# Performance work log

Measured on AMD Instinct MI355X. Metric: run time of the kernel, lower is better.

The kernel has to match this reference:

```python
import jax, jax.numpy as jnp
import numpy as np

H = 16  # n_heads
D = 1024  # embed_dim == input_dim
FF = 4 * D
EPS = 1e-5  # torch LayerNorm default


def layer_norm(x, g, b):
    m = x.mean(-1, keepdims=True)
    v = x.var(-1, keepdims=True)
    return (x - m) / jnp.sqrt(v + EPS) * g + b


def setup_inputs() -> dict:
    key = jax.random.key(0)
    ks = jax.random.split(key, 8)
    s = lambda k, sh: (jax.random.normal(k, sh, jnp.float32) * 0.02)
    return {
        "kq": jax.random.normal(ks[0], (4, 2048, 512), jnp.float32),
        "v": jax.random.normal(ks[1], (4, 2048, 512), jnp.float32),
        "Wk": s(ks[2], (D, D)), "bk": jnp.zeros((D,), jnp.float32),
        "Wq": s(ks[3], (D, D)), "bq": jnp.zeros((D,), jnp.float32),
        "Wv": s(ks[4], (D, D)), "bv": jnp.zeros((D,), jnp.float32),
        "W1": s(ks[5], (FF, D)), "b1": jnp.zeros((FF,), jnp.float32),
        "W2": s(ks[6], (D, FF)), "b2": jnp.zeros((D,), jnp.float32),
        "g1": jnp.ones((D,), jnp.float32), "be1": jnp.zeros((D,), jnp.float32),
        "g2": jnp.ones((D,), jnp.float32), "be2": jnp.zeros((D,), jnp.float32),
    }


def reference(kq, v, Wk, bk, Wq, bq, Wv, bv, W1, b1, W2, b2, g1, be1, g2, be2):
    X = jnp.concatenate([kq, v], axis=-1)  # [n, T, input_dim]
    n, T, _ = kq.shape

    def heads(y):  # [n, T, D] -> [n, H, T, hd]
        return y.reshape(n, T, H, -1).transpose(0, 2, 1, 3)

    K = heads(X @ Wk.T + bk)
    Q = heads(X @ Wq.T + bq)
    V = heads(X @ Wv.T + bv)

    # NOTE: source applies no 1/sqrt(head_dim) scaling
    scores = jnp.einsum('nhqd,nhkd->nhqk', Q, K)
    causal = jnp.tril(jnp.ones((T, T), bool))  # mask = -inf strictly above diagonal
    scores = jnp.where(causal, scores, -jnp.inf)
    A = jax.nn.softmax(scores, axis=-1)
    attn_out = jnp.einsum('nhqk,nhkd->nhqd', A, V)
    attn_out = attn_out.transpose(0, 2, 1, 3).reshape(n, T, -1)  # [n, T, D]

    Vflat = V.transpose(0, 2, 1, 3).reshape(n, T, -1)  # residual is V projection, per source
    h = layer_norm(Vflat + attn_out, g1, be1)
    ff = jax.nn.gelu(h @ W1.T + b1, approximate=False) @ W2.T + b2  # torch GELU default = exact erf
    return layer_norm(h + ff, g2, be2)
```

## Files before the change

### kernel.cpp

```cpp
#include <hip/hip_runtime.h>
#include <stdint.h>

#define SEQ 2048
#define DM  1024
#define NH  16
#define HD  64
#define FFD 4096
#define TOK 8192

typedef __bf16 bf16x8 __attribute__((ext_vector_type(8)));
typedef float  f32x4  __attribute__((ext_vector_type(4)));
typedef float  f32x16 __attribute__((ext_vector_type(16)));
typedef unsigned short u16x8 __attribute__((ext_vector_type(8)));
typedef unsigned short u16x4 __attribute__((ext_vector_type(4)));
typedef unsigned int   u32x4 __attribute__((ext_vector_type(4)));

__device__ __forceinline__ unsigned short f2bf(float f) {
  unsigned u = __builtin_bit_cast(unsigned, f);
  u += 0x7fffu + ((u >> 16) & 1u);
  return (unsigned short)(u >> 16);
}
__device__ __forceinline__ float bf2f(unsigned short h) {
  return __builtin_bit_cast(float, ((unsigned)h) << 16);
}
__device__ __forceinline__ f32x4 mfma16(bf16x8 a, bf16x8 b, f32x4 c) {
  return __builtin_amdgcn_mfma_f32_16x16x32_bf16(a, b, c, 0, 0, 0);
}
__device__ __forceinline__ f32x16 mfma32(bf16x8 a, bf16x8 b, f32x16 c) {
  return __builtin_amdgcn_mfma_f32_32x32x16_bf16(a, b, c, 0, 0, 0);
}
__device__ __forceinline__ unsigned cvtpk(float lo, float hi) {
  unsigned r;
  asm("v_cvt_pk_bf16_f32 %0, %1, %2" : "=v"(r) : "v"(lo), "v"(hi));
  return r;
}
__device__ __forceinline__ void gld_lds16(void* lds, const void* g) {
  __builtin_amdgcn_global_load_lds((__attribute__((address_space(1))) void*)g,
                                   (__attribute__((address_space(3))) void*)lds,
                                   16, 0, 0);
}

__global__ __launch_bounds__(256) void concat_cast(
    const float* __restrict__ kq, const float* __restrict__ v,
    unsigned short* __restrict__ X) {
  int i = (blockIdx.x * 256 + threadIdx.x) * 4;
  int tkn = i >> 10;
  int c = i & 1023;
  const float* s = (c < 512) ? (kq + (size_t)tkn * 512 + c)
                             : (v  + (size_t)tkn * 512 + (c - 512));
  f32x4 f = *(const f32x4*)s;
  u16x4 o = { f2bf(f[0]), f2bf(f[1]), f2bf(f[2]), f2bf(f[3]) };
  *(u16x4*)&X[i] = o;
}

__global__ __launch_bounds__(256) void castW5(
    const float* __restrict__ Wk, const float* __restrict__ Wq,
    const float* __restrict__ Wv, const float* __restrict__ W1,
    const float* __restrict__ W2, unsigned short* __restrict__ dst1,
    unsigned short* __restrict__ dst2) {
  int e = (blockIdx.x * 256 + threadIdx.x) * 4;
  const float* src;
  unsigned short* dst;
  if (e < 3145728) {
    src = (e < 1048576) ? (Wk + e)
        : (e < 2097152) ? (Wq + (e - 1048576))
                        : (Wv + (e - 2097152));
    dst = dst1 + e;
  } else {
    int e2 = e - 3145728;
    src = (e2 < 4194304) ? (W1 + e2) : (W2 + (e2 - 4194304));
    dst = dst2 + e2;
  }
  f32x4 f = *(const f32x4*)src;
  u16x4 o = { f2bf(f[0]), f2bf(f[1]), f2bf(f[2]), f2bf(f[3]) };
  *(u16x4*)dst = o;
}

__global__ __launch_bounds__(256) void bias3(
    const float* __restrict__ a, const float* __restrict__ b,
    const float* __restrict__ c, float* __restrict__ o) {
  int i = blockIdx.x * 256 + threadIdx.x;
  if (i < 1024) o[i] = a[i];
  else if (i < 2048) o[i] = b[i - 1024];
  else if (i < 3072) o[i] = c[i - 2048];
}

template<int BM, int EPI>
__global__ __launch_bounds__(512, 2) void gemm256(
    const unsigned short* __restrict__ A, const unsigned short* __restrict__ B,
    const float* __restrict__ bias, void* __restrict__ Cout,
    void* __restrict__ CoutQ, void* __restrict__ CoutV, void* __restrict__ CoutVI,
    int M, int N, int K, int PR, int PC, int NPC) {
  constexpr int MF = BM / 32;
  constexpr int MG = MF / 4;
  extern __shared__ __align__(16) unsigned short lds[];
  unsigned short* Asm0 = lds;
  unsigned short* Bsm0 = lds + 2 * BM * 64;
  const int tid = threadIdx.x;
  const int w = tid >> 6, l = tid & 63, lr = l & 15, lg = l >> 4;
  const int wm = w >> 2, wn = w & 3;
  const int bid = blockIdx.x;
  const int xcd = bid & 7;
  const int i = bid >> 3;
  const int patch_r = xcd / NPC, patch_c = xcd % NPC;
  const int bm = (patch_r * PR + (i % PR)) * BM;
  const int bn = (patch_c * PC + (i / PR)) * 256;
  const int NT = K >> 6;
  const int srow = tid >> 3;
  const int sc8  = tid & 7;

  f32x4 acc[MF][4] = {};

  auto stage = [&](int kt, int bb) {
    unsigned short* da = Asm0 + bb * (BM * 64);
    unsigned short* db = Bsm0 + bb * (256 * 64);
#pragma unroll
    for (int p = 0; p < BM / 64; ++p) {
      int row = p * 64 + srow;
      gld_lds16(da + (p * 512 + w * 64) * 8,
                &A[(size_t)(bm + row) * K + kt * 64 + ((sc8 ^ (row & 7)) << 3)]);
    }
#pragma unroll
    for (int p = 0; p < 4; ++p) {
      int row = p * 64 + srow;
      gld_lds16(db + (p * 512 + w * 64) * 8,
                &B[(size_t)(bn + row) * K + kt * 64 + ((sc8 ^ (row & 7)) << 3)]);
    }
  };

  stage(0, 0);

  for (int t = 0; t < NT; ++t) {
    asm volatile("s_waitcnt vmcnt(0)" ::: "memory");
    __builtin_amdgcn_s_barrier();
    if (t + 1 < NT) stage(t + 1, (t + 1) & 1);
    const unsigned short* As = Asm0 + (t & 1) * (BM * 64);
    const unsigned short* Bs = Bsm0 + (t & 1) * (256 * 64);
    bf16x8 bv[4][2];
#pragma unroll
    for (int fn = 0; fn < 4; ++fn)
#pragma unroll
      for (int kk = 0; kk < 2; ++kk) {
        int row = wn * 64 + fn * 16 + lr;
        int c8 = (kk * 4 + lg) ^ (row & 7);
        bv[fn][kk] = *(const bf16x8*)&Bs[row * 64 + c8 * 8];
      }
#pragma unroll
    for (int mg = 0; mg < MG; ++mg) {
      bf16x8 av[4][2];
#pragma unroll
      for (int fr = 0; fr < 4; ++fr)
#pragma unroll
        for (int kk = 0; kk < 2; ++kk) {
          int row = wm * (BM / 2) + (mg * 4 + fr) * 16 + lr;
          int c8 = (kk * 4 + lg) ^ (row & 7);
          av[fr][kk] = *(const bf16x8*)&As[row * 64 + c8 * 8];
        }
      __builtin_amdgcn_s_setprio(1);
#pragma unroll
      for (int fr = 0; fr < 4; ++fr)
#pragma unroll
        for (int nf = 0; nf < 4; ++nf)
#pragma unroll
          for (int kk = 0; kk < 2; ++kk)
            acc[mg * 4 + fr][nf] = mfma16(av[fr][kk], bv[nf][kk], acc[mg * 4 + fr][nf]);
      __builtin_amdgcn_s_setprio(0);
    }
  }
#pragma unroll
  for (int mf = 0; mf < MF; ++mf) {
    int row0 = bm + wm * (BM / 2) + mf * 16 + lg * 4;
#pragma unroll
    for (int nf = 0; nf < 4; ++nf) {
      int col = bn + wn * 64 + nf * 16 + lr;
      float bcol = bias[col];
#pragma unroll
      for (int r = 0; r < 4; ++r) {
        float vv = acc[mf][nf][r] + bcol;
        int row = row0 + r;
        if (EPI == 2) vv = 0.5f * vv * (1.0f + erff(vv * 0.70710678118654752f));
        if (EPI == 0) {
          ((float*)Cout)[(size_t)row * N + col] = vv;
        } else if (EPI == 5) {
          int third = col >> 10, c = col & 1023;
          unsigned short hv = f2bf(vv);
          int bb = row >> 11, tt = row & 2047;
          if (third == 0) {
            int hh = c >> 6, dc = (c >> 4) & 3, dl = c & 15;
            ((unsigned short*)Cout)[((((size_t)(bb * 16 + hh) * 4 + dc) * 2048 + tt) << 4) + dl] = hv;
          } else if (third == 1) {
            ((unsigned short*)CoutQ)[(size_t)row * 1024 + c] = hv;
          } else {
            ((unsigned short*)CoutV)[(size_t)row * 1024 + c] = hv;
            int hh = c >> 6, d = c & 63;
            ((unsigned short*)CoutVI)[((((size_t)(bb * 16 + hh) * 128 + (tt >> 4)) * 64 + d) << 4) + (tt & 15)] = hv;
          }
        } else {
          ((unsigned short*)Cout)[(size_t)row * N + col] = f2bf(vv);
        }
      }
    }
  }
}

__global__ __launch_bounds__(128, 4) void attn_kernel(
    const unsigned short* __restrict__ Q, const unsigned short* __restrict__ KI,
    const unsigned short* __restrict__ VI, unsigned short* __restrict__ O) {
  __shared__ __align__(16) unsigned short T[2][32 * 72];
  const int tid = threadIdx.x;
  const int w = tid >> 6, l = tid & 63;
  const int q32 = l & 31;
  const int g = l >> 5;
  const int x = blockIdx.x;
  const int bh = (x & 7) * 8 + (x >> 3);
  const int b = bh >> 4, h = bh & 15;
  const int u = 63 - (2 * (int)blockIdx.y + w);
  const size_t tok0 = (size_t)b * SEQ;
  const size_t hoff = (size_t)h * 64;
  const unsigned short* Kp = KI + (size_t)bh * 4 * SEQ * 16;
  const unsigned short* Vp = VI + (size_t)bh * 128 * 64 * 16;

  const int q0 = u * 32;
  const int qg = q0 + q32;

  bf16x8 qf[4];
#pragma unroll
  for (int ks = 0; ks < 4; ++ks)
    qf[ks] = *(const bf16x8*)&Q[(tok0 + qg) * DM + hoff + ks * 16 + g * 8];

  f32x16 ot0 = {}, ot1 = {};
  float m = -3.0e38f, lden = 0.f;

  bf16x8 kf[4], vf[4];
#pragma unroll
  for (int ks = 0; ks < 4; ++ks)
    kf[ks] = *(const bf16x8*)&Kp[((size_t)ks * SEQ + q32) * 16 + g * 8];
#pragma unroll
  for (int dt = 0; dt < 2; ++dt)
#pragma unroll
    for (int s = 0; s < 2; ++s)
      vf[dt * 2 + s] = *(const bf16x8*)&Vp[((size_t)s * 64 + dt * 32 + q32) * 16 + g * 8];

#pragma unroll 1
  for (int j = 0; j <= u; ++j) {
    f32x16 st = {};
    __builtin_amdgcn_s_setprio(1);
#pragma unroll
    for (int ks = 0; ks < 4; ++ks) st = mfma32(kf[ks], qf[ks], st);
    __builtin_amdgcn_s_setprio(0);
    const int jn = (j < u) ? j + 1 : u;
    bf16x8 kn[4], vn[4];
#pragma unroll
    for (int ks = 0; ks < 4; ++ks)
      kn[ks] = *(const bf16x8*)&Kp[((size_t)ks * SEQ + jn * 32 + q32) * 16 + g * 8];
#pragma unroll
    for (int dt = 0; dt < 2; ++dt)
#pragma unroll
      for (int s = 0; s < 2; ++s)
        vn[dt * 2 + s] = *(const bf16x8*)&Vp[(((size_t)jn * 2 + s) * 64 + dt * 32 + q32) * 16 + g * 8];
    if (j == u) {
#pragma unroll
      for (int r = 0; r < 16; ++r) {
        int kg = j * 32 + (r & 3) + 8 * (r >> 2) + 4 * g;
        if (kg > qg) st[r] = -3.0e38f;
      }
    }
    float x0 = fmaxf(st[0], st[1]),  x1 = fmaxf(st[2], st[3]);
    float x2 = fmaxf(st[4], st[5]),  x3 = fmaxf(st[6], st[7]);
    float x4 = fmaxf(st[8], st[9]),  x5 = fmaxf(st[10], st[11]);
    float x6 = fmaxf(st[12], st[13]), x7 = fmaxf(st[14], st[15]);
    x0 = fmaxf(x0, x1); x2 = fmaxf(x2, x3); x4 = fmaxf(x4, x5); x6 = fmaxf(x6, x7);
    x0 = fmaxf(x0, x2); x4 = fmaxf(x4, x6);
    float pmax = fmaxf(x0, x4);
    if (__any(pmax - m > 8.0f)) {
      float pp = fmaxf(pmax, __shfl_xor(pmax, 32, 64));
      float mnew = fmaxf(m, pp);
      float sc = __expf(m - mnew);
#pragma unroll
      for (int r = 0; r < 16; ++r) { ot0[r] *= sc; ot1[r] *= sc; }
      lden *= sc;
      m = mnew;
    }
    float p[16];
#pragma unroll
    for (int r = 0; r < 16; ++r) p[r] = __expf(st[r] - m);
    {
      float s0 = p[0] + p[1], s1 = p[2] + p[3], s2 = p[4] + p[5], s3 = p[6] + p[7];
      float s4 = p[8] + p[9], s5 = p[10] + p[11], s6 = p[12] + p[13], s7 = p[14] + p[15];
      s0 += s1; s2 += s3; s4 += s5; s6 += s7;
      s0 += s2; s4 += s6;
      lden += s0 + s4;
    }
    unsigned c0 = cvtpk(p[0], p[1]),   c1 = cvtpk(p[2], p[3]);
    unsigned c2 = cvtpk(p[4], p[5]),   c3 = cvtpk(p[6], p[7]);
    unsigned c4 = cvtpk(p[8], p[9]),   c5 = cvtpk(p[10], p[11]);
    unsigned c6 = cvtpk(p[12], p[13]), c7 = cvtpk(p[14], p[15]);
    unsigned y0 = __shfl_xor(c0, 32, 64), y1 = __shfl_xor(c1, 32, 64);
    unsigned y2 = __shfl_xor(c2, 32, 64), y3 = __shfl_xor(c3, 32, 64);
    unsigned y4 = __shfl_xor(c4, 32, 64), y5 = __shfl_xor(c5, 32, 64);
    unsigned y6 = __shfl_xor(c6, 32, 64), y7 = __shfl_xor(c7, 32, 64);
    u32x4 f0 = { g ? y2 : c0, g ? y3 : c1, g ? c2 : y0, g ? c3 : y1 };
    u32x4 f1 = { g ? y6 : c4, g ? y7 : c5, g ? c6 : y4, g ? c7 : y5 };
    bf16x8 pb0 = __builtin_bit_cast(bf16x8, f0);
    bf16x8 pb1 = __builtin_bit_cast(bf16x8, f1);
    __builtin_amdgcn_s_setprio(1);
    ot0 = mfma32(vf[0], pb0, ot0);
    ot0 = mfma32(vf[1], pb1, ot0);
    ot1 = mfma32(vf[2], pb0, ot1);
    ot1 = mfma32(vf[3], pb1, ot1);
    __builtin_amdgcn_s_setprio(0);
#pragma unroll
    for (int ks = 0; ks < 4; ++ks) kf[ks] = kn[ks];
#pragma unroll
    for (int q = 0; q < 4; ++q) vf[q] = vn[q];
  }
  lden += __shfl_xor(lden, 32, 64);
  float inv = 1.0f / lden;
#pragma unroll
  for (int r = 0; r < 16; ++r) {
    int d = (r & 3) + 8 * (r >> 2) + 4 * g;
    T[w][q32 * 72 + d]      = f2bf(ot0[r] * inv);
    T[w][q32 * 72 + 32 + d] = f2bf(ot1[r] * inv);
  }
#pragma unroll
  for (int j2 = 0; j2 < 4; ++j2) {
    int col = g * 32 + j2 * 8;
    u16x8 vv = *(const u16x8*)&T[w][q32 * 72 + col];
    *(u16x8*)&O[(tok0 + q0 + q32) * DM + hoff + col] = vv;
  }
}

template<int MODE>
__global__ __launch_bounds__(256) void ln_kernel(
    const unsigned short* __restrict__ Xa, const void* __restrict__ Xc,
    const float* __restrict__ g, const float* __restrict__ be,
    void* __restrict__ outp) {
  const int row = blockIdx.x, t = threadIdx.x;
  const size_t base = (size_t)row * DM + t * 4;
  float x[4];
  u16x4 a = *(const u16x4*)&Xa[base];
  if (MODE == 0) {
    u16x4 c = *(const u16x4*)&((const unsigned short*)Xc)[base];
#pragma unroll
    for (int i = 0; i < 4; ++i) x[i] = bf2f(a[i]) + bf2f(c[i]);
  } else {
    f32x4 c = *(const f32x4*)&((const float*)Xc)[base];
#pragma unroll
    for (int i = 0; i < 4; ++i) x[i] = bf2f(a[i]) + c[i];
  }
  float s = x[0] + x[1] + x[2] + x[3];
  float ss = x[0] * x[0] + x[1] * x[1] + x[2] * x[2] + x[3] * x[3];
#pragma unroll
  for (int m = 1; m < 64; m <<= 1) {
    s  += __shfl_xor(s, m, 64);
    ss += __shfl_xor(ss, m, 64);
  }
  __shared__ float red[8];
  const int w = t >> 6;
  if ((t & 63) == 0) { red[w * 2] = s; red[w * 2 + 1] = ss; }
  __syncthreads();
  s  = red[0] + red[2] + red[4] + red[6];
  ss = red[1] + red[3] + red[5] + red[7];
  const float mean = s * (1.0f / DM);
  const float var = ss * (1.0f / DM) - mean * mean;
  const float rstd = rsqrtf(var + 1e-5f);
  if (MODE == 0) {
    u16x4 o;
#pragma unroll
    for (int i = 0; i < 4; ++i) {
      int cx = t * 4 + i;
      o[i] = f2bf((x[i] - mean) * rstd * g[cx] + be[cx]);
    }
    *(u16x4*)&((unsigned short*)outp)[base] = o;
  } else {
    f32x4 o;
#pragma unroll
    for (int i = 0; i < 4; ++i) {
      int cx = t * 4 + i;
      o[i] = (x[i] - mean) * rstd * g[cx] + be[cx];
    }
    *(f32x4*)&((float*)outp)[base] = o;
  }
}

extern "C" void kernel_launch(void* const* d_in, const int* in_sizes, int n_in,
                              void* d_out, int out_size, void* d_ws, size_t ws_size,
                              hipStream_t stream) {
  (void)in_sizes; (void)n_in; (void)out_size; (void)ws_size;
  const float* kq  = (const float*)d_in[0];
  const float* v   = (const float*)d_in[1];
  const float* Wk  = (const float*)d_in[2];
  const float* bk  = (const float*)d_in[3];
  const float* Wq  = (const float*)d_in[4];
  const float* bq  = (const float*)d_in[5];
  const float* Wv  = (const float*)d_in[6];
  const float* bv  = (const float*)d_in[7];
  const float* W1  = (const float*)d_in[8];
  const float* b1  = (const float*)d_in[9];
  const float* W2  = (const float*)d_in[10];
  const float* b2  = (const float*)d_in[11];
  const float* g1  = (const float*)d_in[12];
  const float* be1 = (const float*)d_in[13];
  const float* g2  = (const float*)d_in[14];
  const float* be2 = (const float*)d_in[15];
  float* out = (float*)d_out;
  uint8_t* ws = (uint8_t*)d_ws;

  unsigned short* Xb   = (unsigned short*)(ws + 0);
  unsigned short* Wkb  = (unsigned short*)(ws + 16777216);
  unsigned short* Qb   = (unsigned short*)(ws + 23068672);
  unsigned short* Kb   = (unsigned short*)(ws + 39845888);
  unsigned short* Ab   = (unsigned short*)(ws + 56623104);
  unsigned short* F1b  = (unsigned short*)(ws + 0);
  unsigned short* W1b  = (unsigned short*)(ws + 73400320);
  unsigned short* Vb   = (unsigned short*)(ws + 90177536);
  unsigned short* Hb   = (unsigned short*)(ws + 106954752);
  float*          F2f  = (float*)(ws + 123731968);
  unsigned short* VIg  = (unsigned short*)(ws + 123731968);
  float*          bqkv = (float*)(ws + 140509184);
  unsigned short* W2b  = W1b + 4194304;

  concat_cast<<<TOK * DM / 1024, 256, 0, stream>>>(kq, v, Xb);
  castW5<<<11264, 256, 0, stream>>>(Wk, Wq, Wv, W1, W2, Wkb, W1b);
  bias3<<<12, 256, 0, stream>>>(bk, bq, bv, bqkv);

  gemm256<128, 5><<<768, 512, 98304, stream>>>(
      Xb, Wkb, bqkv, Kb, Qb, Vb, VIg, TOK, 3072, DM, 8, 12, 1);

  attn_kernel<<<dim3(64, 32), 128, 0, stream>>>(Qb, Kb, VIg, Ab);

  ln_kernel<0><<<TOK, 256, 0, stream>>>(Vb, Ab, g1, be1, Hb);

  gemm256<256, 2><<<512, 512, 131072, stream>>>(
      Hb, W1b, b1, F1b, nullptr, nullptr, nullptr, TOK, FFD, DM, 8, 8, 2);
  gemm256<128, 0><<<256, 512, 98304, stream>>>(
      F1b, W2b, b2, F2f, nullptr, nullptr, nullptr, TOK, DM, FFD, 8, 4, 1);

  ln_kernel<1><<<TOK, 256, 0, stream>>>(Hb, F2f, g2, be2, out);
}
```

Measured before the change: 369.6 us.

## Split attention KV range across two waves per query tile and merge via LDS

Each block now handles a single 32-query tile, and its two waves each process half of the causal key range. The partial outputs, maxima and denominators are merged through shared memory, with a flash-decoding style rescale. The grid doubles to 64x64 blocks. The goal is better load balance and shorter per-wave critical paths for long causal rows, at the cost of more blocks, extra LDS use, a barrier and duplicated Q loads.

```diff
diff --git a/kernel.cpp b/kernel.cpp
--- a/kernel.cpp
+++ b/kernel.cpp
@@ -206,7 +206,9 @@
 __global__ __launch_bounds__(128, 4) void attn_kernel(
     const unsigned short* __restrict__ Q, const unsigned short* __restrict__ KI,
     const unsigned short* __restrict__ VI, unsigned short* __restrict__ O) {
-  __shared__ __align__(16) unsigned short T[2][32 * 72];
+  __shared__ __align__(16) unsigned short T[32 * 72];
+  __shared__ __align__(16) float O1f[32][68];
+  __shared__ float M1[64], L1[64];
   const int tid = threadIdx.x;
   const int w = tid >> 6, l = tid & 63;
   const int q32 = l & 31;
@@ -214,7 +216,11 @@
   const int x = blockIdx.x;
   const int bh = (x & 7) * 8 + (x >> 3);
   const int b = bh >> 4, h = bh & 15;
-  const int u = 63 - (2 * (int)blockIdx.y + w);
+  const int u = 63 - (int)blockIdx.y;
+  const int nt = u + 1;
+  const int nh = (nt + 1) >> 1;
+  const int jbeg = w ? nh : 0;
+  const int jend = w ? nt : nh;
   const size_t tok0 = (size_t)b * SEQ;
   const size_t hoff = (size_t)h * 64;
   const unsigned short* Kp = KI + (size_t)bh * 4 * SEQ * 16;
@@ -231,102 +237,125 @@
   f32x16 ot0 = {}, ot1 = {};
   float m = -3.0e38f, lden = 0.f;
 
-  bf16x8 kf[4], vf[4];
-#pragma unroll
-  for (int ks = 0; ks < 4; ++ks)
-    kf[ks] = *(const bf16x8*)&Kp[((size_t)ks * SEQ + q32) * 16 + g * 8];
-#pragma unroll
-  for (int dt = 0; dt < 2; ++dt)
-#pragma unroll
-    for (int s = 0; s < 2; ++s)
-      vf[dt * 2 + s] = *(const bf16x8*)&Vp[((size_t)s * 64 + dt * 32 + q32) * 16 + g * 8];
+  if (jbeg < jend) {
+    bf16x8 kf[4], vf[4];
+#pragma unroll
+    for (int ks = 0; ks < 4; ++ks)
+      kf[ks] = *(const bf16x8*)&Kp[((size_t)ks * SEQ + jbeg * 32 + q32) * 16 + g * 8];
+#pragma unroll
+    for (int dt = 0; dt < 2; ++dt)
+#pragma unroll
+      for (int s = 0; s < 2; ++s)
+        vf[dt * 2 + s] = *(const bf16x8*)&Vp[(((size_t)jbeg * 2 + s) * 64 + dt * 32 + q32) * 16 + g * 8];
 
 #pragma unroll 1
-  for (int j = 0; j <= u; ++j) {
-    f32x16 st = {};
-    __builtin_amdgcn_s_setprio(1);
-#pragma unroll
-    for (int ks = 0; ks < 4; ++ks) st = mfma32(kf[ks], qf[ks], st);
-    __builtin_amdgcn_s_setprio(0);
-    const int jn = (j < u) ? j + 1 : u;
-    bf16x8 kn[4], vn[4];
-#pragma unroll
-    for (int ks = 0; ks < 4; ++ks)
-      kn[ks] = *(const bf16x8*)&Kp[((size_t)ks * SEQ + jn * 32 + q32) * 16 + g * 8];
-#pragma unroll
-    for (int dt = 0; dt < 2; ++dt)
-#pragma unroll
-      for (int s = 0; s < 2; ++s)
-        vn[dt * 2 + s] = *(const bf16x8*)&Vp[(((size_t)jn * 2 + s) * 64 + dt * 32 + q32) * 16 + g * 8];
-    if (j == u) {
-#pragma unroll
-      for (int r = 0; r < 16; ++r) {
-        int kg = j * 32 + (r & 3) + 8 * (r >> 2) + 4 * g;
-        if (kg > qg) st[r] = -3.0e38f;
+    for (int j = jbeg; j < jend; ++j) {
+      f32x16 st = {};
+      __builtin_amdgcn_s_setprio(1);
+#pragma unroll
+      for (int ks = 0; ks < 4; ++ks) st = mfma32(kf[ks], qf[ks], st);
+      __builtin_amdgcn_s_setprio(0);
+      const int jn = (j + 1 < jend) ? j + 1 : j;
+      bf16x8 kn[4], vn[4];
+#pragma unroll
+      for (int ks = 0; ks < 4; ++ks)
+        kn[ks] = *(const bf16x8*)&Kp[((size_t)ks * SEQ + jn * 32 + q32) * 16 + g * 8];
+#pragma unroll
+      for (int dt = 0; dt < 2; ++dt)
+#pragma unroll
+        for (int s = 0; s < 2; ++s)
+          vn[dt * 2 + s] = *(const bf16x8*)&Vp[(((size_t)jn * 2 + s) * 64 + dt * 32 + q32) * 16 + g * 8];
+      if (j == u) {
+#pragma unroll
+        for (int r = 0; r < 16; ++r) {
+          int kg = j * 32 + (r & 3) + 8 * (r >> 2) + 4 * g;
+          if (kg > qg) st[r] = -3.0e38f;
+        }
       }
-    }
-    float x0 = fmaxf(st[0], st[1]),  x1 = fmaxf(st[2], st[3]);
-    float x2 = fmaxf(st[4], st[5]),  x3 = fmaxf(st[6], st[7]);
-    float x4 = fmaxf(st[8], st[9]),  x5 = fmaxf(st[10], st[11]);
-    float x6 = fmaxf(st[12], st[13]), x7 = fmaxf(st[14], st[15]);
-    x0 = fmaxf(x0, x1); x2 = fmaxf(x2, x3); x4 = fmaxf(x4, x5); x6 = fmaxf(x6, x7);
-    x0 = fmaxf(x0, x2); x4 = fmaxf(x4, x6);
-    float pmax = fmaxf(x0, x4);
-    if (__any(pmax - m > 8.0f)) {
-      float pp = fmaxf(pmax, __shfl_xor(pmax, 32, 64));
-      float mnew = fmaxf(m, pp);
-      float sc = __expf(m - mnew);
-#pragma unroll
-      for (int r = 0; r < 16; ++r) { ot0[r] *= sc; ot1[r] *= sc; }
-      lden *= sc;
-      m = mnew;
-    }
-    float p[16];
-#pragma unroll
-    for (int r = 0; r < 16; ++r) p[r] = __expf(st[r] - m);
-    {
-      float s0 = p[0] + p[1], s1 = p[2] + p[3], s2 = p[4] + p[5], s3 = p[6] + p[7];
-      float s4 = p[8] + p[9], s5 = p[10] + p[11], s6 = p[12] + p[13], s7 = p[14] + p[15];
-      s0 += s1; s2 += s3; s4 += s5; s6 += s7;
-      s0 += s2; s4 += s6;
-      lden += s0 + s4;
-    }
-    unsigned c0 = cvtpk(p[0], p[1]),   c1 = cvtpk(p[2], p[3]);
-    unsigned c2 = cvtpk(p[4], p[5]),   c3 = cvtpk(p[6], p[7]);
-    unsigned c4 = cvtpk(p[8], p[9]),   c5 = cvtpk(p[10], p[11]);
-    unsigned c6 = cvtpk(p[12], p[13]), c7 = cvtpk(p[14], p[15]);
-    unsigned y0 = __shfl_xor(c0, 32, 64), y1 = __shfl_xor(c1, 32, 64);
-    unsigned y2 = __shfl_xor(c2, 32, 64), y3 = __shfl_xor(c3, 32, 64);
-    unsigned y4 = __shfl_xor(c4, 32, 64), y5 = __shfl_xor(c5, 32, 64);
-    unsigned y6 = __shfl_xor(c6, 32, 64), y7 = __shfl_xor(c7, 32, 64);
-    u32x4 f0 = { g ? y2 : c0, g ? y3 : c1, g ? c2 : y0, g ? c3 : y1 };
-    u32x4 f1 = { g ? y6 : c4, g ? y7 : c5, g ? c6 : y4, g ? c7 : y5 };
-    bf16x8 pb0 = __builtin_bit_cast(bf16x8, f0);
-    bf16x8 pb1 = __builtin_bit_cast(bf16x8, f1);
-    __builtin_amdgcn_s_setprio(1);
-    ot0 = mfma32(vf[0], pb0, ot0);
-    ot0 = mfma32(vf[1], pb1, ot0);
-    ot1 = mfma32(vf[2], pb0, ot1);
-    ot1 = mfma32(vf[3], pb1, ot1);
-    __builtin_amdgcn_s_setprio(0);
-#pragma unroll
-    for (int ks = 0; ks < 4; ++ks) kf[ks] = kn[ks];
-#pragma unroll
-    for (int q = 0; q < 4; ++q) vf[q] = vn[q];
-  }
-  lden += __shfl_xor(lden, 32, 64);
-  float inv = 1.0f / lden;
-#pragma unroll
-  for (int r = 0; r < 16; ++r) {
-    int d = (r & 3) + 8 * (r >> 2) + 4 * g;
-    T[w][q32 * 72 + d]      = f2bf(ot0[r] * inv);
-    T[w][q32 * 72 + 32 + d] = f2bf(ot1[r] * inv);
-  }
-#pragma unroll
-  for (int j2 = 0; j2 < 4; ++j2) {
-    int col = g * 32 + j2 * 8;
-    u16x8 vv = *(const u16x8*)&T[w][q32 * 72 + col];
-    *(u16x8*)&O[(tok0 + q0 + q32) * DM + hoff + col] = vv;
+      float x0 = fmaxf(st[0], st[1]),  x1 = fmaxf(st[2], st[3]);
+      float x2 = fmaxf(st[4], st[5]),  x3 = fmaxf(st[6], st[7]);
+      float x4 = fmaxf(st[8], st[9]),  x5 = fmaxf(st[10], st[11]);
+      float x6 = fmaxf(st[12], st[13]), x7 = fmaxf(st[14], st[15]);
+      x0 = fmaxf(x0, x1); x2 = fmaxf(x2, x3); x4 = fmaxf(x4, x5); x6 = fmaxf(x6, x7);
+      x0 = fmaxf(x0, x2); x4 = fmaxf(x4, x6);
+      float pmax = fmaxf(x0, x4);
+      if (__any(pmax - m > 8.0f)) {
+        float pp = fmaxf(pmax, __shfl_xor(pmax, 32, 64));
+        float mnew = fmaxf(m, pp);
+        float sc = __expf(m - mnew);
+#pragma unroll
+        for (int r = 0; r < 16; ++r) { ot0[r] *= sc; ot1[r] *= sc; }
+        lden *= sc;
+        m = mnew;
+      }
+      float p[16];
+#pragma unroll
+      for (int r = 0; r < 16; ++r) p[r] = __expf(st[r] - m);
+      {
+        float s0 = p[0] + p[1], s1 = p[2] + p[3], s2 = p[4] + p[5], s3 = p[6] + p[7];
+        float s4 = p[8] + p[9], s5 = p[10] + p[11], s6 = p[12] + p[13], s7 = p[14] + p[15];
+        s0 += s1; s2 += s3; s4 += s5; s6 += s7;
+        s0 += s2; s4 += s6;
+        lden += s0 + s4;
+      }
+      unsigned c0 = cvtpk(p[0], p[1]),   c1 = cvtpk(p[2], p[3]);
+      unsigned c2 = cvtpk(p[4], p[5]),   c3 = cvtpk(p[6], p[7]);
+      unsigned c4 = cvtpk(p[8], p[9]),   c5 = cvtpk(p[10], p[11]);
+      unsigned c6 = cvtpk(p[12], p[13]), c7 = cvtpk(p[14], p[15]);
+      unsigned y0 = __shfl_xor(c0, 32, 64), y1 = __shfl_xor(c1, 32, 64);
+      unsigned y2 = __shfl_xor(c2, 32, 64), y3 = __shfl_xor(c3, 32, 64);
+      unsigned y4 = __shfl_xor(c4, 32, 64), y5 = __shfl_xor(c5, 32, 64);
+      unsigned y6 = __shfl_xor(c6, 32, 64), y7 = __shfl_xor(c7, 32, 64);
+      u32x4 f0 = { g ? y2 : c0, g ? y3 : c1, g ? c2 : y0, g ? c3 : y1 };
+      u32x4 f1 = { g ? y6 : c4, g ? y7 : c5, g ? c6 : y4, g ? c7 : y5 };
+      bf16x8 pb0 = __builtin_bit_cast(bf16x8, f0);
+      bf16x8 pb1 = __builtin_bit_cast(bf16x8, f1);
+      __builtin_amdgcn_s_setprio(1);
+      ot0 = mfma32(vf[0], pb0, ot0);
+      ot0 = mfma32(vf[1], pb1, ot0);
+      ot1 = mfma32(vf[2], pb0, ot1);
+      ot1 = mfma32(vf[3], pb1, ot1);
+      __builtin_amdgcn_s_setprio(0);
+#pragma unroll
+      for (int ks = 0; ks < 4; ++ks) kf[ks] = kn[ks];
+#pragma unroll
+      for (int q = 0; q < 4; ++q) vf[q] = vn[q];
+    }
+  }
+  if (w == 1) {
+#pragma unroll
+    for (int r = 0; r < 16; ++r) {
+      O1f[r][l]      = ot0[r];
+      O1f[16 + r][l] = ot1[r];
+    }
+    M1[l] = m;
+    L1[l] = lden;
+  }
+  __syncthreads();
+  if (w == 0) {
+    float m1 = M1[l], l1c = L1[l];
+    float mN = fmaxf(m, m1);
+    float s0 = __expf(m - mN), s1 = __expf(m1 - mN);
+    lden = lden * s0 + l1c * s1;
+    lden += __shfl_xor(lden, 32, 64);
+    float inv = 1.0f / lden;
+#pragma unroll
+    for (int r = 0; r < 16; ++r) {
+      ot0[r] = ot0[r] * s0 + O1f[r][l] * s1;
+      ot1[r] = ot1[r] * s0 + O1f[16 + r][l] * s1;
+    }
+#pragma unroll
+    for (int r = 0; r < 16; ++r) {
+      int d = (r & 3) + 8 * (r >> 2) + 4 * g;
+      T[q32 * 72 + d]      = f2bf(ot0[r] * inv);
+      T[q32 * 72 + 32 + d] = f2bf(ot1[r] * inv);
+    }
+#pragma unroll
+    for (int j2 = 0; j2 < 4; ++j2) {
+      int col = g * 32 + j2 * 8;
+      u16x8 vv = *(const u16x8*)&T[q32 * 72 + col];
+      *(u16x8*)&O[(tok0 + q0 + q32) * DM + hoff + col] = vv;
+    }
   }
 }
 
@@ -427,7 +456,7 @@
   gemm256<128, 5><<<768, 512, 98304, stream>>>(
       Xb, Wkb, bqkv, Kb, Qb, Vb, VIg, TOK, 3072, DM, 8, 12, 1);
 
-  attn_kernel<<<dim3(64, 32), 128, 0, stream>>>(Qb, Kb, VIg, Ab);
+  attn_kernel<<<dim3(64, 64), 128, 0, stream>>>(Qb, Kb, VIg, Ab);
 
   ln_kernel<0><<<TOK, 256, 0, stream>>>(Vb, Ab, g1, be1, Hb);
 
```

After: 368.9 us. About the same (-0.2%).
